# Kernel optimization log

Hardware: AMD Instinct MI355X
Metric: run time of the kernel (lower is better)

Reference implementation:

```python
import jax, jax.numpy as jnp
import numpy as np

N = 4096; E = 32768; S = 64; V = 16; H0 = 64; H1 = 16; STEPS = 3
SQRT3 = float(np.sqrt(3.0))


def _tp(sx, vx, sy, vy):
    # full CG tensor product restricted to paths landing in 0e/1o
    # sx [n,m0], vx [n,m1,3], sy [n,k0], vy [n,k1,3]
    n = sx.shape[0]
    ss = (sx[:, :, None] * sy[:, None, :]).reshape(n, -1)              # 0e x 0e -> 0e
    dd = (jnp.einsum('nmi,nki->nmk', vx, vy) / SQRT3).reshape(n, -1)    # 1o . 1o -> 0e
    sv = (sx[:, :, None, None] * vy[:, None, :, :]).reshape(n, -1, 3)   # 0e x 1o -> 1o
    vs = (vx[:, :, None, :] * sy[:, None, :, None]).reshape(n, -1, 3)   # 1o x 0e -> 1o
    return jnp.concatenate([ss, dd], -1), jnp.concatenate([sv, vs], -2)


def _tpl_gate(sx, vx, sy, vy, ws, b, wv, n0):
    # TensorProductLinearGate: tensor_product -> Linear -> gate
    s_tp, v_tp = _tp(sx, vx, sy, vy)
    s = s_tp @ ws + b                                  # scalars + gate scalars
    v = jnp.einsum('ntd,tm->nmd', v_tp, wv)
    scal = jax.nn.gelu(s[:, :n0])
    gates = jax.nn.sigmoid(s[:, n0:])
    return scal, v * gates[:, :, None]


def _seg_mean(x, idx, n):
    s = jax.ops.segment_sum(x, idx, num_segments=n)
    c = jax.ops.segment_sum(jnp.ones((x.shape[0],), x.dtype), idx, num_segments=n)
    c = jnp.maximum(c, 1.0).reshape((n,) + (1,) * (x.ndim - 1))
    return s / c


def setup_inputs() -> dict:
    key = jax.random.key(0)
    ks = jax.random.split(key, 20)
    f32 = jnp.float32

    def w(k, shape):
        return jax.random.normal(k, shape, f32) / np.sqrt(shape[-2]).astype(np.float32)

    def bias(k, shape):
        return 0.1 * jax.random.normal(k, shape, f32)

    E1 = 2 * (S + V)          # 160: edge block0 TP width
    E2 = H0 + H1              # 80: edge blocks 1-2 TP width
    K0 = H0 + 1; K1 = H1 + 1  # message concat sh
    N0TP = S * K0 + V * K1    # 4432
    N1TP = S * K1 + V * K0    # 2128
    return {
        'node_s': jax.random.normal(ks[0], (N, S), f32),
        'node_v': jax.random.normal(ks[1], (N, V, 3), f32),
        'senders': jax.random.randint(ks[2], (E,), 0, N, jnp.int32),
        'receivers': jax.random.randint(ks[3], (E,), 0, N, jnp.int32),
        'e1_ws': w(ks[4], (STEPS, E1, H0 + H1)),
        'e1_b': bias(ks[5], (STEPS, H0 + H1)),
        'e1_wv': w(ks[6], (STEPS, E1, H1)),
        'e2_ws': w(ks[7], (STEPS, 2, E2, H0 + H1)),
        'e2_b': bias(ks[8], (STEPS, 2, H0 + H1)),
        'e2_wv': w(ks[9], (STEPS, 2, E2, H1)),
        'n_ws': w(ks[10], (STEPS, 3, N0TP, S + V)),
        'n_b': bias(ks[11], (STEPS, 3, S + V)),
        'n_wv': w(ks[12], (STEPS, 3, N1TP, V)),
        'l_ws': w(ks[13], (STEPS, S, S)),
        'l_b': bias(ks[14], (STEPS, S)),
        'l_wv': w(ks[15], (STEPS, V, V)),
    }


def reference(node_s, node_v, senders, receivers, e1_ws, e1_b, e1_wv,
              e2_ws, e2_b, e2_wv, n_ws, n_b, n_wv, l_ws, l_b, l_wv):
    norm = float(E - 1)
    for step in range(STEPS):
        s_i, v_i = node_s[senders], node_v[senders]
        s_j, v_j = node_s[receivers], node_v[receivers]
        r = v_i[:, 0] - v_j[:, 0]                    # slice_by_mul[:1] = positions
        rn = jnp.linalg.norm(r, axis=-1, keepdims=True)
        unit = r / jnp.maximum(rn, 1e-9)
        a_s = jnp.ones((E, 1), node_s.dtype)          # Y_0, component norm
        a_v = (SQRT3 * unit)[:, None, :]              # Y_1, component norm
        m_s = jnp.concatenate([s_i, s_j], -1)
        m_v = jnp.concatenate([v_i, v_j], -2)
        for blk in range(3):
            if blk == 0:
                ws, b, wv = e1_ws[step], e1_b[step], e1_wv[step]
            else:
                ws, b, wv = e2_ws[step, blk - 1], e2_b[step, blk - 1], e2_wv[step, blk - 1]
            m_s, m_v = _tpl_gate(m_s, m_v, a_s, a_v, ws, b, wv, H0)
        # ---- aggregate (segment_mean) + normalize_messages ----
        ms = _seg_mean(m_s, receivers, N) / norm
        mv = _seg_mean(m_v, receivers, N) / norm
        as_ = _seg_mean(a_s, receivers, N) / norm
        av = _seg_mean(a_v, receivers, N) / norm
        y_s = jnp.concatenate([ms, as_], -1)          # [N, H0+1]
        y_v = jnp.concatenate([mv, av], -2)           # [N, H1+1, 3]
        for blk in range(3):
            node_s, node_v = _tpl_gate(node_s, node_v, y_s, y_v,
                                       n_ws[step, blk], n_b[step, blk], n_wv[step, blk], S)
        # ---- final per-step Linear(irreps_in) ----
        node_s = node_s @ l_ws[step] + l_b[step]
        node_v = jnp.einsum('nmd,mk->nkd', node_v, l_wv[step])
    return jnp.concatenate([node_v.reshape(node_v.shape[0], -1), node_s], -1)
```

## Files before the change

kernel.cpp:

```cpp
#include <hip/hip_runtime.h>
#include <math.h>

constexpr int NND = 4096;
constexpr int EDG = 32768;
constexpr float SQRT3  = 1.7320508075688772f;
constexpr float ISQRT3 = 0.5773502691896258f;
constexpr float NORMI  = 1.0f / 32767.0f;

__device__ __forceinline__ float gelu_f(float x) {
    float x3 = x * x * x;
    return 0.5f * x * (1.0f + tanhf(0.7978845608028654f * (x + 0.044715f * x3)));
}
__device__ __forceinline__ float sigmoid_f(float x) {
    return 1.0f / (1.0f + expf(-x));
}

template<int NO4>
__device__ __forceinline__ void rank1(float* acc, float x, const float* w) {
#pragma unroll
    for (int u = 0; u < NO4; ++u) {
        const float4 q = *reinterpret_cast<const float4*>(w + 4 * u);
        acc[4*u+0] = fmaf(x, q.x, acc[4*u+0]);
        acc[4*u+1] = fmaf(x, q.y, acc[4*u+1]);
        acc[4*u+2] = fmaf(x, q.z, acc[4*u+2]);
        acc[4*u+3] = fmaf(x, q.w, acc[4*u+3]);
    }
}

__global__ __launch_bounds__(256)
void segnn_deg_kernel(const int* __restrict__ rcv, int* __restrict__ deg) {
    const int e = blockIdx.x * 256 + threadIdx.x;
    if (e < EDG) atomicAdd(deg + rcv[e], 1);
}

__global__ __launch_bounds__(1024)
void segnn_scan_kernel(const int* __restrict__ deg, int* __restrict__ off) {
    __shared__ int tots[1024];
    const int t = threadIdx.x;
    const int v0 = deg[4*t], v1 = deg[4*t+1], v2 = deg[4*t+2], v3 = deg[4*t+3];
    const int p1 = v0, p2 = p1 + v1, p3 = p2 + v2, p4 = p3 + v3;
    tots[t] = p4;
    __syncthreads();
    for (int d = 1; d < 1024; d <<= 1) {
        const int add = (t >= d) ? tots[t - d] : 0;
        __syncthreads();
        tots[t] += add;
        __syncthreads();
    }
    const int excl = t ? tots[t-1] : 0;
    off[4*t+0] = excl;
    off[4*t+1] = excl + p1;
    off[4*t+2] = excl + p2;
    off[4*t+3] = excl + p3;
    if (t == 1023) off[4096] = tots[1023];
}

__global__ __launch_bounds__(256)
void segnn_scatter_kernel(const int* __restrict__ rcv, const int* __restrict__ off,
                          int* __restrict__ cursor, int* __restrict__ elist) {
    const int e = blockIdx.x * 256 + threadIdx.x;
    if (e < EDG) {
        const int j = rcv[e];
        const int p = atomicAdd(cursor + j, 1);
        elist[off[j] + p] = e;
    }
}

template<int NSX, int NVX>
__device__ __forceinline__ void edge_phase(int e, int h, float ux, float uy, float uz,
                                           const float XS[64][129], const float XV[64][97],
                                           const float* __restrict__ Ws,
                                           const float* __restrict__ B,
                                           const float* __restrict__ Wv,
                                           float* acc, float* accu, float* accv) {
#pragma unroll
    for (int u = 0; u < 20; ++u) acc[u] = B[20*h + u];
#pragma unroll
    for (int u = 0; u < 4; ++u) accu[u] = 0.0f;
#pragma unroll
    for (int u = 0; u < 12; ++u) accv[u] = 0.0f;
    const float* wsr = Ws + 20*h;
    const float* wvr = Wv + 4*h;
#pragma unroll 4
    for (int m = 0; m < NSX; ++m) {
        const float x = XS[e][m];
        rank1<5>(acc,  x, wsr + (size_t)m*80);
        rank1<1>(accu, x, wvr + (size_t)m*16);
    }
#pragma unroll 2
    for (int m = 0; m < NVX; ++m) {
        const float a0 = XV[e][3*m+0], a1 = XV[e][3*m+1], a2 = XV[e][3*m+2];
        const float p = a0*ux + a1*uy + a2*uz;
        rank1<5>(acc, p, wsr + (size_t)(NSX+m)*80);
        const float4 wq = *reinterpret_cast<const float4*>(wvr + (size_t)(NSX+m)*16);
        const float wk[4] = { wq.x, wq.y, wq.z, wq.w };
#pragma unroll
        for (int oo = 0; oo < 4; ++oo) {
            accv[oo*3+0] = fmaf(a0, wk[oo], accv[oo*3+0]);
            accv[oo*3+1] = fmaf(a1, wk[oo], accv[oo*3+1]);
            accv[oo*3+2] = fmaf(a2, wk[oo], accv[oo*3+2]);
        }
    }
}

__global__ __launch_bounds__(256, 2)
void segnn_edge_fused(const float* __restrict__ cs, const float* __restrict__ cv,
                      const int* __restrict__ snd, const int* __restrict__ rcv,
                      const float* __restrict__ W0s, const float* __restrict__ B0, const float* __restrict__ W0v,
                      const float* __restrict__ W1s, const float* __restrict__ B1, const float* __restrict__ W1v,
                      const float* __restrict__ W2s, const float* __restrict__ B2, const float* __restrict__ W2v,
                      float* __restrict__ msg) {
    __shared__ float XS[64][129];
    __shared__ float XV[64][97];
    __shared__ float UU[64][4];
    __shared__ float GG[64][16];

    const int tid = threadIdx.x;
    const int e0  = blockIdx.x * 64;

    for (int idx = tid; idx < 64*128; idx += 256) {
        const int e = idx >> 7, m = idx & 127;
        const int node = (m < 64) ? snd[e0+e] : rcv[e0+e];
        XS[e][m] = cs[(size_t)node*64 + (m & 63)];
    }
    for (int idx = tid; idx < 64*96; idx += 256) {
        const int e = idx / 96, m = idx - e*96;
        const int node = (m < 48) ? snd[e0+e] : rcv[e0+e];
        XV[e][m] = cv[(size_t)node*48 + (m < 48 ? m : m - 48)];
    }
    __syncthreads();
    if (tid < 64) {
        const float rx = XV[tid][0]-XV[tid][48], ry = XV[tid][1]-XV[tid][49], rz = XV[tid][2]-XV[tid][50];
        const float rinv = 1.0f / fmaxf(sqrtf(rx*rx+ry*ry+rz*rz), 1e-9f);
        UU[tid][0] = rx*rinv; UU[tid][1] = ry*rinv; UU[tid][2] = rz*rinv;
    }
    __syncthreads();

    const int e = tid >> 2, h = tid & 3;
    const float ux = UU[e][0], uy = UU[e][1], uz = UU[e][2];
    float acc[20], accu[4], accv[12];

    edge_phase<128,32>(e, h, ux, uy, uz, XS, XV, W0s, B0, W0v, acc, accu, accv);
    __syncthreads();
    if (h == 3) {
#pragma unroll
        for (int u = 0; u < 16; ++u) GG[e][u] = acc[4+u];
    }
    {
        const int ns = (h == 3) ? 4 : 20;
        for (int u = 0; u < ns; ++u) XS[e][20*h + u] = gelu_f(acc[u]);
    }
    __syncthreads();
#pragma unroll
    for (int oo = 0; oo < 4; ++oo) {
        const float g  = sigmoid_f(GG[e][4*h + oo]);
        const float uo = accu[oo] * SQRT3;
        XV[e][(4*h+oo)*3+0] = fmaf(uo, ux, accv[oo*3+0]) * g;
        XV[e][(4*h+oo)*3+1] = fmaf(uo, uy, accv[oo*3+1]) * g;
        XV[e][(4*h+oo)*3+2] = fmaf(uo, uz, accv[oo*3+2]) * g;
    }
    __syncthreads();

    edge_phase<64,16>(e, h, ux, uy, uz, XS, XV, W1s, B1, W1v, acc, accu, accv);
    __syncthreads();
    if (h == 3) {
#pragma unroll
        for (int u = 0; u < 16; ++u) GG[e][u] = acc[4+u];
    }
    {
        const int ns = (h == 3) ? 4 : 20;
        for (int u = 0; u < ns; ++u) XS[e][20*h + u] = gelu_f(acc[u]);
    }
    __syncthreads();
#pragma unroll
    for (int oo = 0; oo < 4; ++oo) {
        const float g  = sigmoid_f(GG[e][4*h + oo]);
        const float uo = accu[oo] * SQRT3;
        XV[e][(4*h+oo)*3+0] = fmaf(uo, ux, accv[oo*3+0]) * g;
        XV[e][(4*h+oo)*3+1] = fmaf(uo, uy, accv[oo*3+1]) * g;
        XV[e][(4*h+oo)*3+2] = fmaf(uo, uz, accv[oo*3+2]) * g;
    }
    __syncthreads();

    edge_phase<64,16>(e, h, ux, uy, uz, XS, XV, W2s, B2, W2v, acc, accu, accv);
    __syncthreads();
    if (h == 3) {
#pragma unroll
        for (int u = 0; u < 16; ++u) GG[e][u] = acc[4+u];
    }
    {
        const int ns = (h == 3) ? 4 : 20;
        for (int u = 0; u < ns; ++u) XS[e][20*h + u] = gelu_f(acc[u]);
    }
    __syncthreads();
#pragma unroll
    for (int oo = 0; oo < 4; ++oo) {
        const float g  = sigmoid_f(GG[e][4*h + oo]);
        const float uo = accu[oo] * SQRT3;
        XV[e][(4*h+oo)*3+0] = fmaf(uo, ux, accv[oo*3+0]) * g;
        XV[e][(4*h+oo)*3+1] = fmaf(uo, uy, accv[oo*3+1]) * g;
        XV[e][(4*h+oo)*3+2] = fmaf(uo, uz, accv[oo*3+2]) * g;
    }
    __syncthreads();
    for (int idx = tid; idx < 64*115; idx += 256) {
        const int e2 = idx / 115, f = idx - e2*115;
        float vv;
        if (f < 64)       vv = XS[e2][f];
        else if (f < 112) vv = XV[e2][f-64];
        else              vv = UU[e2][f-112];
        msg[(size_t)(e0+e2)*116 + f] = vv;
    }
}

__global__ __launch_bounds__(128)
void segnn_gather_kernel(const float* __restrict__ msg, const int* __restrict__ off,
                         const int* __restrict__ elist,
                         float* __restrict__ y_s, float* __restrict__ y_v) {
    const int n = blockIdx.x, f = threadIdx.x;
    const int o0 = off[n], o1 = off[n+1];
    const int deg = o1 - o0;
    float acc = 0.0f;
    for (int p = o0; p < o1; ++p) {
        const int eid = elist[p];
        if (f < 115) acc += msg[(size_t)eid*116 + f];
    }
    const float inv = NORMI / (float)(deg > 0 ? deg : 1);
    if (f < 64)        y_s[(size_t)n*65 + f] = acc * inv;
    else if (f < 112)  y_v[(size_t)n*51 + (f-64)] = acc * inv;
    else if (f < 115)  y_v[(size_t)n*51 + 48 + (f-112)] = SQRT3 * acc * inv;
    else if (f == 115) y_s[(size_t)n*65 + 64] = deg ? NORMI : 0.0f;
}

__global__ __launch_bounds__(512, 4)
void segnn_node_kernel(const float* __restrict__ in_s, const float* __restrict__ in_v,
                       const float* __restrict__ y_s, const float* __restrict__ y_v,
                       const float* __restrict__ W,  const float* __restrict__ B,
                       const float* __restrict__ Wv,
                       float* __restrict__ out_s, float* __restrict__ out_v) {
    __shared__ __align__(16) float xsL[8*65];
    __shared__ __align__(16) float ysL[8*65];
    __shared__ __align__(16) float xvL[8*49];
    __shared__ __align__(16) float yvL[8*51];
    __shared__ __align__(16) float Xa[2][3072];
    __shared__ __align__(16) float red[8][16][40];
    __shared__ float finGG[8*16];

    const int tid  = threadIdx.x;
    const int lane = tid & 63;
    const int wv   = tid >> 6;
    const int nb0  = blockIdx.x * 8;

    for (int idx = tid; idx < 8*64; idx += 512) { const int n = idx >> 6, m = idx & 63; xsL[n*65+m] = in_s[(size_t)(nb0+n)*64 + m]; }
    for (int idx = tid; idx < 8*65; idx += 512) { const int n = idx / 65, k = idx - n*65; ysL[n*65+k] = y_s[(size_t)(nb0+n)*65 + k]; }
    for (int idx = tid; idx < 8*48; idx += 512) { const int n = idx / 48, m = idx - n*48; xvL[n*49+m] = in_v[(size_t)(nb0+n)*48 + m]; }
    for (int idx = tid; idx < 8*51; idx += 512) { const int n = idx / 51, m = idx - n*51; yvL[n*51+m] = y_v[(size_t)(nb0+n)*51 + m]; }
    __syncthreads();

    {
        const int cs = tid & 15;
        const int rowgrp = tid >> 4;

        float acc[8][5];
#pragma unroll
        for (int n = 0; n < 8; ++n)
#pragma unroll
            for (int c = 0; c < 5; ++c) acc[n][c] = 0.0f;

        auto genS = [&](int t, int b) {
            const int base = t * 128;
#pragma unroll
            for (int ii = 0; ii < 2; ++ii) {
                const int idx = tid + ii*512;
                const int rl = idx >> 3, n = idx & 7;
                const int r = base + rl;
                float val = 0.0f;
                if (r < 4160) {
                    const int m = r / 65, k = r - m*65;
                    val = xsL[n*65+m] * ysL[n*65+k];
                } else if (r < 4432) {
                    const int q = r - 4160;
                    const int m = q / 17, k = q - m*17;
                    val = (xvL[n*49+m*3+0]*yvL[n*51+k*3+0] +
                           xvL[n*49+m*3+1]*yvL[n*51+k*3+1] +
                           xvL[n*49+m*3+2]*yvL[n*51+k*3+2]) * ISQRT3;
                }
                Xa[b][idx] = val;
            }
        };

        genS(0, 0);
        __syncthreads();
        for (int t = 0; t < 35; ++t) {
            if (t + 1 < 35) genS(t + 1, (t + 1) & 1);
            const int base = t * 128;
            const float* Xb = &Xa[t & 1][0];
#pragma unroll
            for (int vv = 0; vv < 4; ++vv) {
                const int rl = rowgrp + 32*vv;
                const int r  = base + rl;
                const int wr = r < 4431 ? r : 4431;
                const float* wp = W + (size_t)wr * 80 + cs;
                const float w0 = wp[0], w1 = wp[16], w2 = wp[32], w3 = wp[48], w4_ = wp[64];
                const float4 xq0 = *reinterpret_cast<const float4*>(&Xb[rl*8]);
                const float4 xq1 = *reinterpret_cast<const float4*>(&Xb[rl*8+4]);
                const float xn[8] = { xq0.x, xq0.y, xq0.z, xq0.w, xq1.x, xq1.y, xq1.z, xq1.w };
#pragma unroll
                for (int n = 0; n < 8; ++n) {
                    acc[n][0] = fmaf(xn[n], w0,  acc[n][0]);
                    acc[n][1] = fmaf(xn[n], w1,  acc[n][1]);
                    acc[n][2] = fmaf(xn[n], w2,  acc[n][2]);
                    acc[n][3] = fmaf(xn[n], w3,  acc[n][3]);
                    acc[n][4] = fmaf(xn[n], w4_, acc[n][4]);
                }
            }
            __syncthreads();
        }

#pragma unroll
        for (int n = 0; n < 8; ++n)
#pragma unroll
            for (int c = 0; c < 5; ++c) {
                float a = acc[n][c];
                a += __shfl_xor(a, 16);
                a += __shfl_xor(a, 32);
                if (lane < 16) red[wv][lane][n*5+c] = a;
            }
        __syncthreads();
        for (int idx = tid; idx < 8*80; idx += 512) {
            const int n = idx / 80, col = idx - n*80;
            const int cs2 = col & 15, ci2 = col >> 4;
            float s = B[col];
#pragma unroll
            for (int w = 0; w < 8; ++w) s += red[w][cs2][n*5+ci2];
            if (col < 64) out_s[(size_t)(nb0+n)*64 + col] = gelu_f(s);
            else          finGG[n*16 + (col-64)] = s;
        }
    }

    {
        const int j4 = tid & 3;
        const int ngrp = (tid >> 2) & 1;
        const int rg = tid >> 3;

        float av[12][4];
#pragma unroll
        for (int a = 0; a < 12; ++a)
#pragma unroll
            for (int c = 0; c < 4; ++c) av[a][c] = 0.0f;

        auto genV = [&](int t, int b) {
            const int base = t * 128;
#pragma unroll
            for (int ii = 0; ii < 6; ++ii) {
                const int idx = tid + ii*512;
                const int rl = idx / 24, ar = idx - rl*24;
                const int n = ar / 3, d = ar - n*3;
                const int r = base + rl;
                float val = 0.0f;
                if (r < 1088) {
                    const int m = r / 17, k = r - m*17;
                    val = xsL[n*65+m] * yvL[n*51+k*3+d];
                } else if (r < 2128) {
                    const int q = r - 1088;
                    const int m = q / 65, k = q - m*65;
                    val = xvL[n*49+m*3+d] * ysL[n*65+k];
                }
                Xa[b][idx] = val;
            }
        };

        genV(0, 0);
        __syncthreads();
        for (int t = 0; t < 17; ++t) {
            if (t + 1 < 17) genV(t + 1, (t + 1) & 1);
            const int base = t * 128;
            const float* Xb = &Xa[t & 1][0];
#pragma unroll
            for (int vv = 0; vv < 2; ++vv) {
                const int rl = rg + 64*vv;
                const int r  = base + rl;
                const int wr = r < 2127 ? r : 2127;
                const float4 w4 = *reinterpret_cast<const float4*>(&Wv[(size_t)wr*16 + 4*j4]);
                const float4 xq0 = *reinterpret_cast<const float4*>(&Xb[rl*24 + 12*ngrp]);
                const float4 xq1 = *reinterpret_cast<const float4*>(&Xb[rl*24 + 12*ngrp + 4]);
                const float4 xq2 = *reinterpret_cast<const float4*>(&Xb[rl*24 + 12*ngrp + 8]);
                const float xr[12] = { xq0.x,xq0.y,xq0.z,xq0.w, xq1.x,xq1.y,xq1.z,xq1.w, xq2.x,xq2.y,xq2.z,xq2.w };
#pragma unroll
                for (int a = 0; a < 12; ++a) {
                    av[a][0] = fmaf(xr[a], w4.x, av[a][0]);
                    av[a][1] = fmaf(xr[a], w4.y, av[a][1]);
                    av[a][2] = fmaf(xr[a], w4.z, av[a][2]);
                    av[a][3] = fmaf(xr[a], w4.w, av[a][3]);
                }
            }
            __syncthreads();
        }

        float* redf = &red[0][0][0];
#pragma unroll
        for (int a = 0; a < 12; ++a)
#pragma unroll
            for (int c = 0; c < 4; ++c) {
                float x = av[a][c];
                x += __shfl_xor(x, 8);
                x += __shfl_xor(x, 16);
                x += __shfl_xor(x, 32);
                if (lane < 8) redf[wv*384 + lane*48 + a*4 + c] = x;
            }
        __syncthreads();
        for (int idx = tid; idx < 24*16; idx += 512) {
            const int ar = idx >> 4, j = idx & 15;
            const int n = ar / 3, d = ar - n*3;
            const int ng2 = ar / 12, a2 = ar - 12*ng2;
            const int jj4 = j >> 2, c2 = j & 3;
            float s = 0.0f;
#pragma unroll
            for (int w = 0; w < 8; ++w) s += redf[w*384 + (jj4 + 4*ng2)*48 + a2*4 + c2];
            out_v[(size_t)(nb0+n)*48 + j*3 + d] = s * sigmoid_f(finGG[n*16 + j]);
        }
    }
}

__global__ __launch_bounds__(256)
void segnn_linear_kernel(const float* __restrict__ in_s, const float* __restrict__ in_v,
                         const float* __restrict__ lws, const float* __restrict__ lb,
                         const float* __restrict__ lwv,
                         float* __restrict__ out_s, float* __restrict__ out_v,
                         float* __restrict__ out_cat) {
    const int idx = blockIdx.x * 256 + threadIdx.x;
    if (idx >= NND * 112) return;
    const int nidx = idx / 112, f = idx - nidx * 112;
    if (f < 48) {
        const int k = f / 3, d = f - 3*k;
        const float* vp = in_v + (size_t)nidx * 48 + d;
        float acc = 0.0f;
#pragma unroll
        for (int m = 0; m < 16; ++m) acc = fmaf(vp[m*3], lwv[m*16 + k], acc);
        if (out_cat) out_cat[(size_t)nidx*112 + f] = acc;
        else         out_v[(size_t)nidx*48 + f] = acc;
    } else {
        const int o = f - 48;
        const float* sp = in_s + (size_t)nidx * 64;
        float acc = lb[o];
#pragma unroll
        for (int m = 0; m < 64; ++m) acc = fmaf(sp[m], lws[m*64 + o], acc);
        if (out_cat) out_cat[(size_t)nidx*112 + f] = acc;
        else         out_s[(size_t)nidx*64 + o] = acc;
    }
}

extern "C" void kernel_launch(void* const* d_in, const int* in_sizes, int n_in,
                              void* d_out, int out_size, void* d_ws, size_t ws_size,
                              hipStream_t stream) {
    const float* in_s  = (const float*)d_in[0];
    const float* in_v  = (const float*)d_in[1];
    const int*   snd   = (const int*)  d_in[2];
    const int*   rcv   = (const int*)  d_in[3];
    const float* e1_ws = (const float*)d_in[4];
    const float* e1_b  = (const float*)d_in[5];
    const float* e1_wv = (const float*)d_in[6];
    const float* e2_ws = (const float*)d_in[7];
    const float* e2_b  = (const float*)d_in[8];
    const float* e2_wv = (const float*)d_in[9];
    const float* n_ws  = (const float*)d_in[10];
    const float* n_b   = (const float*)d_in[11];
    const float* n_wv  = (const float*)d_in[12];
    const float* l_ws  = (const float*)d_in[13];
    const float* l_b   = (const float*)d_in[14];
    const float* l_wv  = (const float*)d_in[15];

    float* ws    = (float*)d_ws;
    float* cur_s = ws;
    float* cur_v = cur_s + 262144;
    float* nxt_s = cur_v + 196608;
    float* nxt_v = nxt_s + 262144;
    float* y_s   = nxt_v + 196608;
    float* y_v   = y_s + 266240;
    float* msg   = y_v + 208896;
    int*   deg    = (int*)(msg + 3801088);
    int*   cursor = deg + 4096;
    int*   off    = cursor + 4096;
    int*   elist  = off + 4097;

    hipMemsetAsync(deg, 0, (size_t)8192 * sizeof(int), stream);
    hipMemcpyAsync(cur_s, in_s, (size_t)262144 * sizeof(float), hipMemcpyDeviceToDevice, stream);
    hipMemcpyAsync(cur_v, in_v, (size_t)196608 * sizeof(float), hipMemcpyDeviceToDevice, stream);
    segnn_deg_kernel<<<EDG/256, 256, 0, stream>>>(rcv, deg);
    segnn_scan_kernel<<<1, 1024, 0, stream>>>(deg, off);
    segnn_scatter_kernel<<<EDG/256, 256, 0, stream>>>(rcv, off, cursor, elist);

    for (int step = 0; step < 3; ++step) {
        segnn_edge_fused<<<EDG/64, 256, 0, stream>>>(cur_s, cur_v, snd, rcv,
            e1_ws + (size_t)step*160*80, e1_b + step*80, e1_wv + (size_t)step*160*16,
            e2_ws + (size_t)(step*2+0)*80*80, e2_b + (step*2+0)*80, e2_wv + (size_t)(step*2+0)*80*16,
            e2_ws + (size_t)(step*2+1)*80*80, e2_b + (step*2+1)*80, e2_wv + (size_t)(step*2+1)*80*16,
            msg);
        segnn_gather_kernel<<<NND, 128, 0, stream>>>(msg, off, elist, y_s, y_v);

        segnn_node_kernel<<<NND/8, 512, 0, stream>>>(cur_s, cur_v, y_s, y_v,
            n_ws + (size_t)(step*3+0)*4432*80, n_b + (step*3+0)*80, n_wv + (size_t)(step*3+0)*2128*16,
            nxt_s, nxt_v);
        segnn_node_kernel<<<NND/8, 512, 0, stream>>>(nxt_s, nxt_v, y_s, y_v,
            n_ws + (size_t)(step*3+1)*4432*80, n_b + (step*3+1)*80, n_wv + (size_t)(step*3+1)*2128*16,
            cur_s, cur_v);
        segnn_node_kernel<<<NND/8, 512, 0, stream>>>(cur_s, cur_v, y_s, y_v,
            n_ws + (size_t)(step*3+2)*4432*80, n_b + (step*3+2)*80, n_wv + (size_t)(step*3+2)*2128*16,
            nxt_s, nxt_v);

        segnn_linear_kernel<<<(NND*112 + 255)/256, 256, 0, stream>>>(nxt_s, nxt_v,
            l_ws + (size_t)step*64*64, l_b + step*64, l_wv + (size_t)step*16*16,
            cur_s, cur_v, (step == 2) ? (float*)d_out : nullptr);
    }
}
```

Baseline: 1.258 ms.

## Restructure edge MLP as tiled GEMM over 16-edge blocks with split-K reduction

Rewrites the fused edge kernel to process 16 edges per block with transposed shared-memory inputs. Each thread now owns one column slice for 8 edges across a split K range, so weight loads are reused across edges instead of every edge thread streaming the full weight matrix. Partial sums are combined with cross-lane shuffles and a shared-memory reduction. This adds extra barriers and reduction traffic, and the grid grows four times larger with a higher occupancy hint.

New measurement: 1.181 ms. -6.1%, faster.

```diff
diff --git a/kernel.cpp b/kernel.cpp
--- a/kernel.cpp
+++ b/kernel.cpp
@@ -67,148 +67,221 @@
 }
 
 template<int NSX, int NVX>
-__device__ __forceinline__ void edge_phase(int e, int h, float ux, float uy, float uz,
-                                           const float XS[64][129], const float XV[64][97],
-                                           const float* __restrict__ Ws,
-                                           const float* __restrict__ B,
-                                           const float* __restrict__ Wv,
-                                           float* acc, float* accu, float* accv) {
-#pragma unroll
-    for (int u = 0; u < 20; ++u) acc[u] = B[20*h + u];
-#pragma unroll
-    for (int u = 0; u < 4; ++u) accu[u] = 0.0f;
-#pragma unroll
-    for (int u = 0; u < 12; ++u) accv[u] = 0.0f;
-    const float* wsr = Ws + 20*h;
-    const float* wvr = Wv + 4*h;
-#pragma unroll 4
-    for (int m = 0; m < NSX; ++m) {
-        const float x = XS[e][m];
-        rank1<5>(acc,  x, wsr + (size_t)m*80);
-        rank1<1>(accu, x, wvr + (size_t)m*16);
-    }
+__device__ __forceinline__ void edge_gemm_phase(
+    const int tid,
+    const float* __restrict__ Ws, const float* __restrict__ Bs,
+    const float* __restrict__ Wv,
+    const float (*XT)[20], const float (*X2T)[20],
+    float (*red)[16][8][6], float (*Cbuf)[96], float (*Cv)[48])
+{
+    const int cs   = tid & 15;
+    const int rgl  = (tid >> 4) & 3;
+    const int wvw  = tid >> 6;
+    const int eg   = wvw & 1;
+    const int kh   = wvw >> 1;
+    const int lane = tid & 63;
+    constexpr int KA = NSX + NVX;
+    constexpr int CH = KA / 8;
+
+    {
+        float acc[8][6];
+#pragma unroll
+        for (int j = 0; j < 8; ++j)
+#pragma unroll
+            for (int c = 0; c < 6; ++c) acc[j][c] = 0.0f;
+        const int r0 = (kh*4 + rgl) * CH;
 #pragma unroll 2
-    for (int m = 0; m < NVX; ++m) {
-        const float a0 = XV[e][3*m+0], a1 = XV[e][3*m+1], a2 = XV[e][3*m+2];
-        const float p = a0*ux + a1*uy + a2*uz;
-        rank1<5>(acc, p, wsr + (size_t)(NSX+m)*80);
-        const float4 wq = *reinterpret_cast<const float4*>(wvr + (size_t)(NSX+m)*16);
-        const float wk[4] = { wq.x, wq.y, wq.z, wq.w };
-#pragma unroll
-        for (int oo = 0; oo < 4; ++oo) {
-            accv[oo*3+0] = fmaf(a0, wk[oo], accv[oo*3+0]);
-            accv[oo*3+1] = fmaf(a1, wk[oo], accv[oo*3+1]);
-            accv[oo*3+2] = fmaf(a2, wk[oo], accv[oo*3+2]);
-        }
-    }
-}
-
-__global__ __launch_bounds__(256, 2)
+        for (int rr = 0; rr < CH; ++rr) {
+            const int r = r0 + rr;
+            const float* wp = Ws + r*80 + cs;
+            const float w0 = wp[0], w1 = wp[16], w2 = wp[32], w3 = wp[48], w4 = wp[64];
+            const float w5 = (r < NSX) ? Wv[r*16 + cs] : 0.0f;
+            const float4 xa = *reinterpret_cast<const float4*>(&XT[r][8*eg]);
+            const float4 xb = *reinterpret_cast<const float4*>(&XT[r][8*eg+4]);
+            const float xe[8] = { xa.x,xa.y,xa.z,xa.w, xb.x,xb.y,xb.z,xb.w };
+#pragma unroll
+            for (int j = 0; j < 8; ++j) {
+                acc[j][0] = fmaf(xe[j], w0, acc[j][0]);
+                acc[j][1] = fmaf(xe[j], w1, acc[j][1]);
+                acc[j][2] = fmaf(xe[j], w2, acc[j][2]);
+                acc[j][3] = fmaf(xe[j], w3, acc[j][3]);
+                acc[j][4] = fmaf(xe[j], w4, acc[j][4]);
+                acc[j][5] = fmaf(xe[j], w5, acc[j][5]);
+            }
+        }
+#pragma unroll
+        for (int j = 0; j < 8; ++j)
+#pragma unroll
+            for (int c = 0; c < 6; ++c) {
+                float a = acc[j][c];
+                a += __shfl_xor(a, 16);
+                a += __shfl_xor(a, 32);
+                acc[j][c] = a;
+            }
+        if (lane < 16) {
+#pragma unroll
+            for (int j = 0; j < 8; ++j)
+#pragma unroll
+                for (int c = 0; c < 6; ++c) red[wvw][lane][j][c] = acc[j][c];
+        }
+    }
+    __syncthreads();
+    for (int idx = tid; idx < 16*96; idx += 256) {
+        const int e = idx / 96, col = idx - e*96;
+        const int eg2 = e >> 3, j = e & 7;
+        const int cs2 = col & 15, ci = col >> 4;
+        float s = red[eg2][cs2][j][ci] + red[2+eg2][cs2][j][ci];
+        if (col < 80) s += Bs[col];
+        Cbuf[e][col] = s;
+    }
+    __syncthreads();
+
+    {
+        constexpr int CHB = NVX / 8;
+        float av[8][3];
+#pragma unroll
+        for (int j = 0; j < 8; ++j) { av[j][0]=0.0f; av[j][1]=0.0f; av[j][2]=0.0f; }
+        const int m0 = (kh*4 + rgl) * CHB;
+#pragma unroll
+        for (int mm = 0; mm < CHB; ++mm) {
+            const int m = m0 + mm;
+            const float w = Wv[(NSX + m)*16 + cs];
+#pragma unroll
+            for (int d = 0; d < 3; ++d) {
+                const float4 xa = *reinterpret_cast<const float4*>(&X2T[d*NVX + m][8*eg]);
+                const float4 xb = *reinterpret_cast<const float4*>(&X2T[d*NVX + m][8*eg+4]);
+                const float xe[8] = { xa.x,xa.y,xa.z,xa.w, xb.x,xb.y,xb.z,xb.w };
+#pragma unroll
+                for (int j = 0; j < 8; ++j) av[j][d] = fmaf(xe[j], w, av[j][d]);
+            }
+        }
+#pragma unroll
+        for (int j = 0; j < 8; ++j)
+#pragma unroll
+            for (int d = 0; d < 3; ++d) {
+                float a = av[j][d];
+                a += __shfl_xor(a, 16);
+                a += __shfl_xor(a, 32);
+                av[j][d] = a;
+            }
+        if (lane < 16) {
+#pragma unroll
+            for (int j = 0; j < 8; ++j)
+#pragma unroll
+                for (int d = 0; d < 3; ++d) red[wvw][lane][j][d] = av[j][d];
+        }
+    }
+    __syncthreads();
+    for (int idx = tid; idx < 16*48; idx += 256) {
+        const int e = idx / 48, q = idx - e*48;
+        const int o = q / 3, d = q - 3*o;
+        const int eg2 = e >> 3, j = e & 7;
+        Cv[e][q] = red[eg2][o][j][d] + red[2+eg2][o][j][d];
+    }
+    __syncthreads();
+}
+
+__global__ __launch_bounds__(256, 3)
 void segnn_edge_fused(const float* __restrict__ cs, const float* __restrict__ cv,
                       const int* __restrict__ snd, const int* __restrict__ rcv,
                       const float* __restrict__ W0s, const float* __restrict__ B0, const float* __restrict__ W0v,
                       const float* __restrict__ W1s, const float* __restrict__ B1, const float* __restrict__ W1v,
                       const float* __restrict__ W2s, const float* __restrict__ B2, const float* __restrict__ W2v,
                       float* __restrict__ msg) {
-    __shared__ float XS[64][129];
-    __shared__ float XV[64][97];
-    __shared__ float UU[64][4];
-    __shared__ float GG[64][16];
+    __shared__ __align__(16) float XT[160][20];
+    __shared__ __align__(16) float X2T[96][20];
+    __shared__ float red[4][16][8][6];
+    __shared__ float Cbuf[16][96];
+    __shared__ float Cv[16][48];
+    __shared__ float uu[16][4];
+    __shared__ int   nd[16][2];
 
     const int tid = threadIdx.x;
-    const int e0  = blockIdx.x * 64;
-
-    for (int idx = tid; idx < 64*128; idx += 256) {
+    const int e0  = blockIdx.x * 16;
+
+    if (tid < 16) { nd[tid][0] = snd[e0+tid]; nd[tid][1] = rcv[e0+tid]; }
+    __syncthreads();
+    for (int idx = tid; idx < 16*128; idx += 256) {
         const int e = idx >> 7, m = idx & 127;
-        const int node = (m < 64) ? snd[e0+e] : rcv[e0+e];
-        XS[e][m] = cs[(size_t)node*64 + (m & 63)];
-    }
-    for (int idx = tid; idx < 64*96; idx += 256) {
-        const int e = idx / 96, m = idx - e*96;
-        const int node = (m < 48) ? snd[e0+e] : rcv[e0+e];
-        XV[e][m] = cv[(size_t)node*48 + (m < 48 ? m : m - 48)];
-    }
-    __syncthreads();
-    if (tid < 64) {
-        const float rx = XV[tid][0]-XV[tid][48], ry = XV[tid][1]-XV[tid][49], rz = XV[tid][2]-XV[tid][50];
+        const int node = nd[e][m >> 6];
+        XT[m][e] = cs[(size_t)node*64 + (m & 63)];
+    }
+    for (int idx = tid; idx < 16*96; idx += 256) {
+        const int e = idx / 96, q = idx - e*96;
+        const int part = q / 48, md = q - part*48;
+        const int m = md / 3, d = md - m*3;
+        const int node = nd[e][part];
+        X2T[d*32 + part*16 + m][e] = cv[(size_t)node*48 + m*3 + d];
+    }
+    __syncthreads();
+    if (tid < 16) {
+        const float rx = X2T[0][tid]  - X2T[16][tid];
+        const float ry = X2T[32][tid] - X2T[48][tid];
+        const float rz = X2T[64][tid] - X2T[80][tid];
         const float rinv = 1.0f / fmaxf(sqrtf(rx*rx+ry*ry+rz*rz), 1e-9f);
-        UU[tid][0] = rx*rinv; UU[tid][1] = ry*rinv; UU[tid][2] = rz*rinv;
-    }
-    __syncthreads();
-
-    const int e = tid >> 2, h = tid & 3;
-    const float ux = UU[e][0], uy = UU[e][1], uz = UU[e][2];
-    float acc[20], accu[4], accv[12];
-
-    edge_phase<128,32>(e, h, ux, uy, uz, XS, XV, W0s, B0, W0v, acc, accu, accv);
-    __syncthreads();
-    if (h == 3) {
-#pragma unroll
-        for (int u = 0; u < 16; ++u) GG[e][u] = acc[4+u];
-    }
-    {
-        const int ns = (h == 3) ? 4 : 20;
-        for (int u = 0; u < ns; ++u) XS[e][20*h + u] = gelu_f(acc[u]);
-    }
-    __syncthreads();
-#pragma unroll
-    for (int oo = 0; oo < 4; ++oo) {
-        const float g  = sigmoid_f(GG[e][4*h + oo]);
-        const float uo = accu[oo] * SQRT3;
-        XV[e][(4*h+oo)*3+0] = fmaf(uo, ux, accv[oo*3+0]) * g;
-        XV[e][(4*h+oo)*3+1] = fmaf(uo, uy, accv[oo*3+1]) * g;
-        XV[e][(4*h+oo)*3+2] = fmaf(uo, uz, accv[oo*3+2]) * g;
-    }
-    __syncthreads();
-
-    edge_phase<64,16>(e, h, ux, uy, uz, XS, XV, W1s, B1, W1v, acc, accu, accv);
-    __syncthreads();
-    if (h == 3) {
-#pragma unroll
-        for (int u = 0; u < 16; ++u) GG[e][u] = acc[4+u];
-    }
-    {
-        const int ns = (h == 3) ? 4 : 20;
-        for (int u = 0; u < ns; ++u) XS[e][20*h + u] = gelu_f(acc[u]);
-    }
-    __syncthreads();
-#pragma unroll
-    for (int oo = 0; oo < 4; ++oo) {
-        const float g  = sigmoid_f(GG[e][4*h + oo]);
-        const float uo = accu[oo] * SQRT3;
-        XV[e][(4*h+oo)*3+0] = fmaf(uo, ux, accv[oo*3+0]) * g;
-        XV[e][(4*h+oo)*3+1] = fmaf(uo, uy, accv[oo*3+1]) * g;
-        XV[e][(4*h+oo)*3+2] = fmaf(uo, uz, accv[oo*3+2]) * g;
-    }
-    __syncthreads();
-
-    edge_phase<64,16>(e, h, ux, uy, uz, XS, XV, W2s, B2, W2v, acc, accu, accv);
-    __syncthreads();
-    if (h == 3) {
-#pragma unroll
-        for (int u = 0; u < 16; ++u) GG[e][u] = acc[4+u];
-    }
-    {
-        const int ns = (h == 3) ? 4 : 20;
-        for (int u = 0; u < ns; ++u) XS[e][20*h + u] = gelu_f(acc[u]);
-    }
-    __syncthreads();
-#pragma unroll
-    for (int oo = 0; oo < 4; ++oo) {
-        const float g  = sigmoid_f(GG[e][4*h + oo]);
-        const float uo = accu[oo] * SQRT3;
-        XV[e][(4*h+oo)*3+0] = fmaf(uo, ux, accv[oo*3+0]) * g;
-        XV[e][(4*h+oo)*3+1] = fmaf(uo, uy, accv[oo*3+1]) * g;
-        XV[e][(4*h+oo)*3+2] = fmaf(uo, uz, accv[oo*3+2]) * g;
-    }
-    __syncthreads();
-    for (int idx = tid; idx < 64*115; idx += 256) {
-        const int e2 = idx / 115, f = idx - e2*115;
+        uu[tid][0] = rx*rinv; uu[tid][1] = ry*rinv; uu[tid][2] = rz*rinv;
+    }
+    __syncthreads();
+    for (int idx = tid; idx < 16*32; idx += 256) {
+        const int e = idx >> 5, mm = idx & 31;
+        XT[128 + mm][e] = X2T[mm][e]*uu[e][0] + X2T[32+mm][e]*uu[e][1] + X2T[64+mm][e]*uu[e][2];
+    }
+    __syncthreads();
+
+    edge_gemm_phase<128,32>(tid, W0s, B0, W0v, XT, X2T, red, Cbuf, Cv);
+    for (int idx = tid; idx < 16*64; idx += 256) {
+        const int e = idx >> 6, m = idx & 63;
+        XT[m][e] = gelu_f(Cbuf[e][m]);
+    }
+    for (int idx = tid; idx < 16*16; idx += 256) {
+        const int e = idx >> 4, o = idx & 15;
+        const float g = sigmoid_f(Cbuf[e][64+o]);
+        const float t = Cbuf[e][80+o] * SQRT3;
+        float p = 0.0f;
+#pragma unroll
+        for (int d = 0; d < 3; ++d) {
+            const float vd = fmaf(t, uu[e][d], Cv[e][o*3+d]) * g;
+            X2T[d*16 + o][e] = vd;
+            p = fmaf(vd, uu[e][d], p);
+        }
+        XT[64 + o][e] = p;
+    }
+    __syncthreads();
+
+    edge_gemm_phase<64,16>(tid, W1s, B1, W1v, XT, X2T, red, Cbuf, Cv);
+    for (int idx = tid; idx < 16*64; idx += 256) {
+        const int e = idx >> 6, m = idx & 63;
+        XT[m][e] = gelu_f(Cbuf[e][m]);
+    }
+    for (int idx = tid; idx < 16*16; idx += 256) {
+        const int e = idx >> 4, o = idx & 15;
+        const float g = sigmoid_f(Cbuf[e][64+o]);
+        const float t = Cbuf[e][80+o] * SQRT3;
+        float p = 0.0f;
+#pragma unroll
+        for (int d = 0; d < 3; ++d) {
+            const float vd = fmaf(t, uu[e][d], Cv[e][o*3+d]) * g;
+            X2T[d*16 + o][e] = vd;
+            p = fmaf(vd, uu[e][d], p);
+        }
+        XT[64 + o][e] = p;
+    }
+    __syncthreads();
+
+    edge_gemm_phase<64,16>(tid, W2s, B2, W2v, XT, X2T, red, Cbuf, Cv);
+    for (int idx = tid; idx < 16*115; idx += 256) {
+        const int e = idx / 115, f = idx - e*115;
         float vv;
-        if (f < 64)       vv = XS[e2][f];
-        else if (f < 112) vv = XV[e2][f-64];
-        else              vv = UU[e2][f-112];
-        msg[(size_t)(e0+e2)*116 + f] = vv;
+        if (f < 64) {
+            vv = gelu_f(Cbuf[e][f]);
+        } else if (f < 112) {
+            const int q = f - 64, o = q / 3, d = q - 3*o;
+            const float g = sigmoid_f(Cbuf[e][64+o]);
+            vv = fmaf(Cbuf[e][80+o] * SQRT3, uu[e][d], Cv[e][q]) * g;
+        } else {
+            vv = uu[e][f-112];
+        }
+        msg[(size_t)(e0+e)*116 + f] = vv;
     }
 }
 
@@ -490,7 +563,7 @@
     segnn_scatter_kernel<<<EDG/256, 256, 0, stream>>>(rcv, off, cursor, elist);
 
     for (int step = 0; step < 3; ++step) {
-        segnn_edge_fused<<<EDG/64, 256, 0, stream>>>(cur_s, cur_v, snd, rcv,
+        segnn_edge_fused<<<EDG/16, 256, 0, stream>>>(cur_s, cur_v, snd, rcv,
             e1_ws + (size_t)step*160*80, e1_b + step*80, e1_wv + (size_t)step*160*16,
             e2_ws + (size_t)(step*2+0)*80*80, e2_b + (step*2+0)*80, e2_wv + (size_t)(step*2+0)*80*16,
             e2_ws + (size_t)(step*2+1)*80*80, e2_b + (step*2+1)*80, e2_wv + (size_t)(step*2+1)*80*16,
```
